# Kernel tuning notes

Measured on AMD Instinct MI355X. Metric: run time of the kernel, lower is better.

The kernel has to match this reference:

```python
import jax, jax.numpy as jnp
import numpy as np

DECAY = 0.99
EPSILON = 1e-05
CODEBOOK_SIZE = 1024


def setup_inputs() -> dict:
    key = jax.random.key(0)
    k1, k2, k3 = jax.random.split(key, 3)
    B, T, D, K = 8, 4096, 128, CODEBOOK_SIZE
    return {
        "x": jax.random.normal(k1, (B, T, D), dtype=jnp.float32),
        "embed": jax.random.normal(k2, (K, D), dtype=jnp.float32),
        "cluster_size": jnp.ones((K,), dtype=jnp.float32),
        "embed_avg": jax.random.normal(k3, (K, D), dtype=jnp.float32),
    }


def reference(x, embed, cluster_size, embed_avg):
    shape = x.shape
    K, D = embed.shape
    flat = x.reshape(-1, D)  # (N, D)

    dist = 2.0 * (flat @ embed.T) - jnp.sum(flat * flat, axis=1, keepdims=True) \
           - jnp.sum(embed * embed, axis=1)[None, :]  # (N, K)
    embed_ind_flat = jnp.argmax(dist, axis=-1)  # (N,) int
    embed_ind = embed_ind_flat.reshape(shape[:-1])
    quantize = embed[embed_ind]  # dequantize via gather, (B, T, D)

    # training EMA updates (one-hot scatter expressed as segment sums)
    counts = jax.ops.segment_sum(jnp.ones_like(embed_ind_flat, dtype=x.dtype),
                                 embed_ind_flat, num_segments=K)  # == onehot.sum(0)
    embed_sum = jax.ops.segment_sum(flat, embed_ind_flat, num_segments=K)  # == (x.T @ onehot).T

    new_cluster_size = cluster_size * DECAY + (1.0 - DECAY) * counts
    new_embed_avg = embed_avg * DECAY + (1.0 - DECAY) * embed_sum

    total = new_cluster_size.sum()
    smoothed = (new_cluster_size + EPSILON) / (total + K * EPSILON) * total
    new_embed = new_embed_avg / smoothed[:, None]

    return quantize, embed_ind, new_cluster_size, new_embed_avg, new_embed
```

## Files before the change

kernel.cpp:

```cpp
#include <hip/hip_runtime.h>

#define NROWS 32768
#define DDIM  128
#define KCODES 1024
#define DECAY 0.99f
#define OMD   0.01f
#define EPS   1e-5f

typedef __attribute__((ext_vector_type(8))) short short8;
typedef __attribute__((ext_vector_type(4))) float f32x4;

#define WS_COUNTS 0
#define WS_OFFS   1024
#define WS_CURSOR 2048
#define WS_INV    3072
#define WS_EN2H   4096
#define WS_BUCKET 5120

__device__ __forceinline__ unsigned int f2bf(float f) {
  union { float f; unsigned int u; } cv; cv.f = f;
  unsigned int u = cv.u;
  return (u + 0x7fffu + ((u >> 16) & 1u)) >> 16;
}

__global__ __launch_bounds__(256) void pack_e(const float* __restrict__ embed,
                                              ushort* __restrict__ epack,
                                              float* __restrict__ en2h) {
  const int tid = threadIdx.x;
  const int w = tid >> 6, lane = tid & 63;
  const int nt = blockIdx.x * 4 + w;
  const int m = lane & 15, q = lane >> 4;
  const int row = nt * 16 + m;
  const float* ep = embed + (size_t)row * DDIM + q * 8;
  float ss = 0.f;
  #pragma unroll
  for (int kb = 0; kb < 4; ++kb) {
    float4 v0 = *(const float4*)(ep + kb * 32);
    float4 v1 = *(const float4*)(ep + kb * 32 + 4);
    float v[8] = {v0.x, v0.y, v0.z, v0.w, v1.x, v1.y, v1.z, v1.w};
    unsigned int h[8], l[8];
    #pragma unroll
    for (int j = 0; j < 8; ++j) {
      ss += v[j] * v[j];
      h[j] = f2bf(v[j]);
      float fh = __uint_as_float(h[j] << 16);
      l[j] = f2bf(v[j] - fh);
    }
    uint4 ph, pl;
    ph.x = h[0] | (h[1] << 16); ph.y = h[2] | (h[3] << 16);
    ph.z = h[4] | (h[5] << 16); ph.w = h[6] | (h[7] << 16);
    pl.x = l[0] | (l[1] << 16); pl.y = l[2] | (l[3] << 16);
    pl.z = l[4] | (l[5] << 16); pl.w = l[6] | (l[7] << 16);
    *(uint4*)(epack + (((size_t)nt * 8 + kb) * 64 + lane) * 8)     = ph;
    *(uint4*)(epack + (((size_t)nt * 8 + kb + 4) * 64 + lane) * 8) = pl;
  }
  ss += __shfl_xor(ss, 16, 64);
  ss += __shfl_xor(ss, 32, 64);
  if (q == 0) en2h[row] = 0.5f * ss;
}

__global__ __launch_bounds__(256) void vq_mfma(
    const float* __restrict__ x, const short8* __restrict__ ep8,
    const float* __restrict__ en2h, const float* __restrict__ embed,
    float* __restrict__ out_ind, float* __restrict__ out_q) {
  __shared__ unsigned long long keys[4][32];
  __shared__ int scodes[32];
  const int tid = threadIdx.x;
  const int w = tid >> 6, lane = tid & 63;
  const int c = lane & 15, q = lane >> 4;
  const int mt0 = blockIdx.x * 2;

  short8 a[2][8];
  #pragma unroll
  for (int t = 0; t < 2; ++t) {
    const float* xp = x + (size_t)((mt0 + t) * 16 + c) * DDIM + q * 8;
    #pragma unroll
    for (int kb = 0; kb < 4; ++kb) {
      float4 v0 = *(const float4*)(xp + kb * 32);
      float4 v1 = *(const float4*)(xp + kb * 32 + 4);
      float v[8] = {v0.x, v0.y, v0.z, v0.w, v1.x, v1.y, v1.z, v1.w};
      short8 hh, ll;
      #pragma unroll
      for (int j = 0; j < 8; ++j) {
        unsigned int hv = f2bf(v[j]);
        hh[j] = (short)hv;
        float fh = __uint_as_float(hv << 16);
        ll[j] = (short)f2bf(v[j] - fh);
      }
      a[t][kb] = hh;
      a[t][kb + 4] = ll;
    }
  }

  float bestv[8]; int besti[8];
  #pragma unroll
  for (int i = 0; i < 8; ++i) { bestv[i] = -3.4e38f; besti[i] = 0; }

  const int nt0 = w * 16;
  for (int ch = 0; ch < 16; ++ch) {
    const int nt = nt0 + ch;
    short8 st[8];
    #pragma unroll
    for (int j = 0; j < 8; ++j)
      st[j] = ep8[((size_t)nt * 8 + j) * 64 + lane];
    const float nh = en2h[nt * 16 + c];
    f32x4 acc0 = {0.f, 0.f, 0.f, 0.f}, acc1 = {0.f, 0.f, 0.f, 0.f};
    #pragma unroll
    for (int kb = 0; kb < 4; ++kb) {
      acc0 = __builtin_amdgcn_mfma_f32_16x16x32_bf16(a[0][kb], st[kb], acc0, 0, 0, 0);
      acc1 = __builtin_amdgcn_mfma_f32_16x16x32_bf16(a[1][kb], st[kb], acc1, 0, 0, 0);
    }
    #pragma unroll
    for (int kb = 0; kb < 4; ++kb) {
      acc0 = __builtin_amdgcn_mfma_f32_16x16x32_bf16(a[0][kb + 4], st[kb], acc0, 0, 0, 0);
      acc1 = __builtin_amdgcn_mfma_f32_16x16x32_bf16(a[1][kb + 4], st[kb], acc1, 0, 0, 0);
    }
    #pragma unroll
    for (int kb = 0; kb < 4; ++kb) {
      acc0 = __builtin_amdgcn_mfma_f32_16x16x32_bf16(a[0][kb], st[kb + 4], acc0, 0, 0, 0);
      acc1 = __builtin_amdgcn_mfma_f32_16x16x32_bf16(a[1][kb], st[kb + 4], acc1, 0, 0, 0);
    }
    const int code = nt * 16 + c;
    #pragma unroll
    for (int r = 0; r < 4; ++r) {
      float s0 = acc0[r] - nh;
      if (s0 > bestv[r])     { bestv[r] = s0;     besti[r] = code; }
      float s1 = acc1[r] - nh;
      if (s1 > bestv[4 + r]) { bestv[4 + r] = s1; besti[4 + r] = code; }
    }
  }

  #pragma unroll
  for (int off = 1; off < 16; off <<= 1) {
    #pragma unroll
    for (int i = 0; i < 8; ++i) {
      float ov = __shfl_xor(bestv[i], off, 64);
      int   oi = __shfl_xor(besti[i], off, 64);
      if (ov > bestv[i] || (ov == bestv[i] && oi < besti[i])) {
        bestv[i] = ov; besti[i] = oi;
      }
    }
  }
  if (c == 0) {
    #pragma unroll
    for (int t = 0; t < 2; ++t)
      #pragma unroll
      for (int r = 0; r < 4; ++r) {
        unsigned u = __float_as_uint(bestv[t * 4 + r]);
        unsigned su = (u & 0x80000000u) ? ~u : (u | 0x80000000u);
        keys[w][t * 16 + q * 4 + r] =
            ((unsigned long long)su << 32) |
            (unsigned long long)(0xFFFFFFFFu - (unsigned)besti[t * 4 + r]);
      }
  }
  __syncthreads();
  if (tid < 32) {
    unsigned long long k0 = keys[0][tid], k1 = keys[1][tid];
    unsigned long long k2 = keys[2][tid], k3 = keys[3][tid];
    unsigned long long k = k0 > k1 ? k0 : k1;
    if (k2 > k) k = k2;
    if (k3 > k) k = k3;
    int code = (int)(0xFFFFFFFFu - (unsigned)(k & 0xFFFFFFFFull));
    out_ind[blockIdx.x * 32 + tid] = (float)code;
    scodes[tid] = code;
  }
  __syncthreads();
  #pragma unroll
  for (int it = 0; it < 4; ++it) {
    int idx = tid + it * 256;
    int row = idx >> 5, c4 = idx & 31;
    int code = scodes[row];
    *(float4*)(out_q + (size_t)(blockIdx.x * 32 + row) * DDIM + c4 * 4) =
        *(const float4*)(embed + (size_t)code * DDIM + c4 * 4);
  }
}

__global__ __launch_bounds__(1024) void scan_fin(
    const float* __restrict__ out_ind, const float* __restrict__ cs,
    float* __restrict__ counts_g, int* __restrict__ offs, int* __restrict__ cursor,
    float* __restrict__ inv, float* __restrict__ out_ncs) {
  __shared__ int hist[1024];
  __shared__ float wtot[16], ctot[16];
  const int tid = threadIdx.x;
  const int lane = tid & 63, w = tid >> 6;
  hist[tid] = 0;
  __syncthreads();
  #pragma unroll
  for (int i = 0; i < 32; ++i)
    atomicAdd(&hist[(int)out_ind[i * 1024 + tid]], 1);
  __syncthreads();
  const int cnt = hist[tid];
  const float cnum = (float)cnt;
  const float cv = cs[tid];
  float s = cnum;
  #pragma unroll
  for (int off = 1; off < 64; off <<= 1) {
    float v = __shfl_up(s, off, 64);
    if (lane >= off) s += v;
  }
  float r2 = cv;
  #pragma unroll
  for (int off = 32; off > 0; off >>= 1) r2 += __shfl_down(r2, off, 64);
  if (lane == 63) wtot[w] = s;
  if (lane == 0)  ctot[w] = r2;
  __syncthreads();
  if (tid < 16) {
    float v = wtot[tid];
    #pragma unroll
    for (int off = 1; off < 16; off <<= 1) {
      float p = __shfl_up(v, off, 64);
      if (tid >= off) v += p;
    }
    wtot[tid] = v;
    float t2 = ctot[tid];
    #pragma unroll
    for (int off = 8; off > 0; off >>= 1) t2 += __shfl_down(t2, off, 64);
    if (tid == 0) ctot[0] = t2;
  }
  __syncthreads();
  const float prefix = (w > 0) ? wtot[w - 1] : 0.f;
  const int excl = (int)(s + prefix) - cnt;
  offs[tid] = excl;
  cursor[tid] = excl;
  counts_g[tid] = cnum;
  const float ncs = cv * DECAY + OMD * cnum;
  out_ncs[tid] = ncs;
  const float total = ctot[0] * DECAY + OMD * (float)NROWS;
  inv[tid] = (total + (float)KCODES * EPS) / ((ncs + EPS) * total);
}

__global__ void scatter_rows(const float* __restrict__ out_ind,
                             int* __restrict__ cursor, int* __restrict__ bucket) {
  int row = blockIdx.x * 256 + threadIdx.x;
  int code = (int)out_ind[row];
  int pos = atomicAdd(cursor + code, 1);
  bucket[pos] = row;
}

__global__ __launch_bounds__(256) void esum_fin(
    const int* __restrict__ bucket, const int* __restrict__ offs,
    const float* __restrict__ counts, const float* __restrict__ x,
    const float* __restrict__ ea, const float* __restrict__ inv,
    float* __restrict__ out_nea, float* __restrict__ out_ne) {
  __shared__ float4 part[512];
  const int code = blockIdx.x;
  const int t = threadIdx.x;
  const int c8 = t & 15;
  const int h = t >> 4;
  const int start = offs[code];
  const int cnt = (int)counts[code];
  float4 a0 = {0.f, 0.f, 0.f, 0.f}, a1 = {0.f, 0.f, 0.f, 0.f};
  int i = h;
  for (; i + 16 < cnt; i += 32) {
    int rowA = bucket[start + i];
    int rowB = bucket[start + i + 16];
    const float* pa = x + (size_t)rowA * DDIM + c8 * 8;
    const float* pb = x + (size_t)rowB * DDIM + c8 * 8;
    float4 xa0 = *(const float4*)(pa), xa1 = *(const float4*)(pa + 4);
    float4 xb0 = *(const float4*)(pb), xb1 = *(const float4*)(pb + 4);
    a0.x += xa0.x + xb0.x; a0.y += xa0.y + xb0.y; a0.z += xa0.z + xb0.z; a0.w += xa0.w + xb0.w;
    a1.x += xa1.x + xb1.x; a1.y += xa1.y + xb1.y; a1.z += xa1.z + xb1.z; a1.w += xa1.w + xb1.w;
  }
  for (; i < cnt; i += 16) {
    int row = bucket[start + i];
    const float* pa = x + (size_t)row * DDIM + c8 * 8;
    float4 xa0 = *(const float4*)(pa), xa1 = *(const float4*)(pa + 4);
    a0.x += xa0.x; a0.y += xa0.y; a0.z += xa0.z; a0.w += xa0.w;
    a1.x += xa1.x; a1.y += xa1.y; a1.z += xa1.z; a1.w += xa1.w;
  }
  part[h * 32 + c8 * 2]     = a0;
  part[h * 32 + c8 * 2 + 1] = a1;
  __syncthreads();
  if (t < 32) {
    float4 s = part[t];
    #pragma unroll
    for (int hh = 1; hh < 16; ++hh) {
      float4 p = part[hh * 32 + t];
      s.x += p.x; s.y += p.y; s.z += p.z; s.w += p.w;
    }
    float iv = inv[code];
    int base = code * DDIM + t * 4;
    float4 a = *(const float4*)(ea + base);
    float4 nea;
    nea.x = a.x * DECAY + OMD * s.x; nea.y = a.y * DECAY + OMD * s.y;
    nea.z = a.z * DECAY + OMD * s.z; nea.w = a.w * DECAY + OMD * s.w;
    *(float4*)(out_nea + base) = nea;
    float4 ne;
    ne.x = nea.x * iv; ne.y = nea.y * iv; ne.z = nea.z * iv; ne.w = nea.w * iv;
    *(float4*)(out_ne + base) = ne;
  }
}

extern "C" void kernel_launch(void* const* d_in, const int* in_sizes, int n_in,
                              void* d_out, int out_size, void* d_ws, size_t ws_size,
                              hipStream_t stream) {
  const float* x     = (const float*)d_in[0];
  const float* embed = (const float*)d_in[1];
  const float* cs    = (const float*)d_in[2];
  const float* ea    = (const float*)d_in[3];

  float* out     = (float*)d_out;
  float* out_q   = out;
  float* out_ind = out_q + 4194304;
  float* out_ncs = out_ind + 32768;
  float* out_nea = out_ncs + 1024;
  float* out_ne  = out_nea + 131072;

  float* ws     = (float*)d_ws;
  float* counts = ws + WS_COUNTS;
  int*   offs   = (int*)(ws + WS_OFFS);
  int*   cursor = (int*)(ws + WS_CURSOR);
  float* inv    = ws + WS_INV;
  float* en2h   = ws + WS_EN2H;
  int*   bucket = (int*)(ws + WS_BUCKET);

  ushort* epack = (ushort*)out_nea;

  pack_e<<<16, 256, 0, stream>>>(embed, epack, en2h);
  vq_mfma<<<NROWS / 32, 256, 0, stream>>>(x, (const short8*)epack, en2h, embed,
                                          out_ind, out_q);
  scan_fin<<<1, 1024, 0, stream>>>(out_ind, cs, counts, offs, cursor, inv, out_ncs);
  scatter_rows<<<NROWS / 256, 256, 0, stream>>>(out_ind, cursor, bucket);
  esum_fin<<<KCODES, 256, 0, stream>>>(bucket, offs, counts, x, ea, inv,
                                       out_nea, out_ne);
}
```

Measured before the change: 170.2 us.

## Double-buffer codebook loads in VQ MFMA loop and fuse histogram via global atomics

Software-pipelines the codebook tile loads in the MFMA argmax loop with two register buffers, sched barriers and s_setprio around the MFMA block. The accumulator is now initialised with the negative half-norm, which drops a subtraction per element. The per-code histogram moves out of the single-block scan kernel into global atomics issued by the VQ kernel, with pack_e zeroing the counts. This removes the serial 32K-element shared-memory histogram pass, at the cost of contended global atomics and extra register pressure.

```diff
diff --git a/kernel.cpp b/kernel.cpp
--- a/kernel.cpp
+++ b/kernel.cpp
@@ -25,8 +25,13 @@
 
 __global__ __launch_bounds__(256) void pack_e(const float* __restrict__ embed,
                                               ushort* __restrict__ epack,
-                                              float* __restrict__ en2h) {
+                                              float* __restrict__ en2h,
+                                              int* __restrict__ cnt0) {
   const int tid = threadIdx.x;
+  if (blockIdx.x == 0) {
+    #pragma unroll
+    for (int i = 0; i < 4; ++i) cnt0[tid + i * 256] = 0;
+  }
   const int w = tid >> 6, lane = tid & 63;
   const int nt = blockIdx.x * 4 + w;
   const int m = lane & 15, q = lane >> 4;
@@ -62,7 +67,8 @@
 __global__ __launch_bounds__(256) void vq_mfma(
     const float* __restrict__ x, const short8* __restrict__ ep8,
     const float* __restrict__ en2h, const float* __restrict__ embed,
-    float* __restrict__ out_ind, float* __restrict__ out_q) {
+    float* __restrict__ out_ind, float* __restrict__ out_q,
+    int* __restrict__ cnt_i) {
   __shared__ unsigned long long keys[4][32];
   __shared__ int scodes[32];
   const int tid = threadIdx.x;
@@ -97,14 +103,13 @@
   for (int i = 0; i < 8; ++i) { bestv[i] = -3.4e38f; besti[i] = 0; }
 
   const int nt0 = w * 16;
-  for (int ch = 0; ch < 16; ++ch) {
-    const int nt = nt0 + ch;
-    short8 st[8];
-    #pragma unroll
-    for (int j = 0; j < 8; ++j)
-      st[j] = ep8[((size_t)nt * 8 + j) * 64 + lane];
-    const float nh = en2h[nt * 16 + c];
-    f32x4 acc0 = {0.f, 0.f, 0.f, 0.f}, acc1 = {0.f, 0.f, 0.f, 0.f};
+  const short8* pb = ep8 + (size_t)nt0 * 8 * 64 + lane;
+  const float* pn = en2h + nt0 * 16 + c;
+
+  auto proc = [&](const short8 (&st)[8], float nh, int nt) {
+    f32x4 acc0 = {-nh, -nh, -nh, -nh};
+    f32x4 acc1 = acc0;
+    __builtin_amdgcn_s_setprio(1);
     #pragma unroll
     for (int kb = 0; kb < 4; ++kb) {
       acc0 = __builtin_amdgcn_mfma_f32_16x16x32_bf16(a[0][kb], st[kb], acc0, 0, 0, 0);
@@ -120,15 +125,42 @@
       acc0 = __builtin_amdgcn_mfma_f32_16x16x32_bf16(a[0][kb], st[kb + 4], acc0, 0, 0, 0);
       acc1 = __builtin_amdgcn_mfma_f32_16x16x32_bf16(a[1][kb], st[kb + 4], acc1, 0, 0, 0);
     }
+    __builtin_amdgcn_s_setprio(0);
     const int code = nt * 16 + c;
     #pragma unroll
     for (int r = 0; r < 4; ++r) {
-      float s0 = acc0[r] - nh;
-      if (s0 > bestv[r])     { bestv[r] = s0;     besti[r] = code; }
-      float s1 = acc1[r] - nh;
-      if (s1 > bestv[4 + r]) { bestv[4 + r] = s1; besti[4 + r] = code; }
-    }
-  }
+      if (acc0[r] > bestv[r])     { bestv[r] = acc0[r];     besti[r] = code; }
+      if (acc1[r] > bestv[4 + r]) { bestv[4 + r] = acc1[r]; besti[4 + r] = code; }
+    }
+  };
+
+  short8 sA[8], sB[8];
+  float nhA, nhB;
+  #pragma unroll
+  for (int j = 0; j < 8; ++j) sA[j] = pb[j * 64];
+  nhA = pn[0];
+
+  for (int ch = 0; ch < 14; ch += 2) {
+    pb += 512;
+    #pragma unroll
+    for (int j = 0; j < 8; ++j) sB[j] = pb[j * 64];
+    nhB = pn[16 * (ch + 1)];
+    __builtin_amdgcn_sched_barrier(0);
+    proc(sA, nhA, nt0 + ch);
+    pb += 512;
+    #pragma unroll
+    for (int j = 0; j < 8; ++j) sA[j] = pb[j * 64];
+    nhA = pn[16 * (ch + 2)];
+    __builtin_amdgcn_sched_barrier(0);
+    proc(sB, nhB, nt0 + ch + 1);
+  }
+  pb += 512;
+  #pragma unroll
+  for (int j = 0; j < 8; ++j) sB[j] = pb[j * 64];
+  nhB = pn[16 * 15];
+  __builtin_amdgcn_sched_barrier(0);
+  proc(sA, nhA, nt0 + 14);
+  proc(sB, nhB, nt0 + 15);
 
   #pragma unroll
   for (int off = 1; off < 16; off <<= 1) {
@@ -163,6 +195,7 @@
     int code = (int)(0xFFFFFFFFu - (unsigned)(k & 0xFFFFFFFFull));
     out_ind[blockIdx.x * 32 + tid] = (float)code;
     scodes[tid] = code;
+    atomicAdd(&cnt_i[code], 1);
   }
   __syncthreads();
   #pragma unroll
@@ -176,20 +209,13 @@
 }
 
 __global__ __launch_bounds__(1024) void scan_fin(
-    const float* __restrict__ out_ind, const float* __restrict__ cs,
-    float* __restrict__ counts_g, int* __restrict__ offs, int* __restrict__ cursor,
+    int* offs, const float* __restrict__ cs,
+    float* __restrict__ counts_g, int* __restrict__ cursor,
     float* __restrict__ inv, float* __restrict__ out_ncs) {
-  __shared__ int hist[1024];
   __shared__ float wtot[16], ctot[16];
   const int tid = threadIdx.x;
   const int lane = tid & 63, w = tid >> 6;
-  hist[tid] = 0;
-  __syncthreads();
-  #pragma unroll
-  for (int i = 0; i < 32; ++i)
-    atomicAdd(&hist[(int)out_ind[i * 1024 + tid]], 1);
-  __syncthreads();
-  const int cnt = hist[tid];
+  const int cnt = offs[tid];
   const float cnum = (float)cnt;
   const float cv = cs[tid];
   float s = cnum;
@@ -316,10 +342,10 @@
 
   ushort* epack = (ushort*)out_nea;
 
-  pack_e<<<16, 256, 0, stream>>>(embed, epack, en2h);
+  pack_e<<<16, 256, 0, stream>>>(embed, epack, en2h, offs);
   vq_mfma<<<NROWS / 32, 256, 0, stream>>>(x, (const short8*)epack, en2h, embed,
-                                          out_ind, out_q);
-  scan_fin<<<1, 1024, 0, stream>>>(out_ind, cs, counts, offs, cursor, inv, out_ncs);
+                                          out_ind, out_q, offs);
+  scan_fin<<<1, 1024, 0, stream>>>(offs, cs, counts, cursor, inv, out_ncs);
   scatter_rows<<<NROWS / 256, 256, 0, stream>>>(out_ind, cursor, bucket);
   esum_fin<<<KCODES, 256, 0, stream>>>(bucket, offs, counts, x, ea, inv,
                                        out_nea, out_ne);
```

Result: faster. 161.2 us (-5.3%).

## Restructure VQ kernel to stage codebook in LDS and fuse histogram

Applied to the files above, without the earlier changes.

The nearest-code kernel now uses 512-thread blocks covering 128 rows. Each wave holds one 16-row A tile and sweeps all 1024 codes instead of splitting codes across waves. Codebook fragments are double-buffered into LDS via global_load_lds, and the half-norms are staged in LDS and folded into the accumulator init. The three split-bf16 MFMA chains are interleaved into independent accumulators, and the cross-wave argmax reduction disappears. Code counts are now accumulated with global atomics in the VQ kernel, zeroed in pack_e, which removes the single-block histogram pass in scan_fin but adds per-iteration barriers and atomic contention.

```diff
diff --git a/kernel.cpp b/kernel.cpp
--- a/kernel.cpp
+++ b/kernel.cpp
@@ -23,57 +23,72 @@
   return (u + 0x7fffu + ((u >> 16) & 1u)) >> 16;
 }
 
+__device__ __forceinline__ void gload16(const void* g, void* l) {
+  __builtin_amdgcn_global_load_lds(
+      (const __attribute__((address_space(1))) unsigned int*)g,
+      (__attribute__((address_space(3))) unsigned int*)l, 16, 0, 0);
+}
+
 __global__ __launch_bounds__(256) void pack_e(const float* __restrict__ embed,
                                               ushort* __restrict__ epack,
-                                              float* __restrict__ en2h) {
+                                              float* __restrict__ en2h,
+                                              int* __restrict__ cnt0) {
   const int tid = threadIdx.x;
-  const int w = tid >> 6, lane = tid & 63;
-  const int nt = blockIdx.x * 4 + w;
-  const int m = lane & 15, q = lane >> 4;
+  const int nt = blockIdx.x;
+  if (nt == 0) {
+    #pragma unroll
+    for (int i = 0; i < 4; ++i) cnt0[tid + i * 256] = 0;
+  }
+  const int m = tid >> 4, s = tid & 15;
+  const int kb = s >> 2, q = s & 3;
   const int row = nt * 16 + m;
-  const float* ep = embed + (size_t)row * DDIM + q * 8;
+  const float* ep = embed + (size_t)row * DDIM + kb * 32 + q * 8;
+  float4 v0 = *(const float4*)(ep);
+  float4 v1 = *(const float4*)(ep + 4);
+  float v[8] = {v0.x, v0.y, v0.z, v0.w, v1.x, v1.y, v1.z, v1.w};
+  unsigned int h[8], l[8];
   float ss = 0.f;
   #pragma unroll
-  for (int kb = 0; kb < 4; ++kb) {
-    float4 v0 = *(const float4*)(ep + kb * 32);
-    float4 v1 = *(const float4*)(ep + kb * 32 + 4);
-    float v[8] = {v0.x, v0.y, v0.z, v0.w, v1.x, v1.y, v1.z, v1.w};
-    unsigned int h[8], l[8];
-    #pragma unroll
-    for (int j = 0; j < 8; ++j) {
-      ss += v[j] * v[j];
-      h[j] = f2bf(v[j]);
-      float fh = __uint_as_float(h[j] << 16);
-      l[j] = f2bf(v[j] - fh);
-    }
-    uint4 ph, pl;
-    ph.x = h[0] | (h[1] << 16); ph.y = h[2] | (h[3] << 16);
-    ph.z = h[4] | (h[5] << 16); ph.w = h[6] | (h[7] << 16);
-    pl.x = l[0] | (l[1] << 16); pl.y = l[2] | (l[3] << 16);
-    pl.z = l[4] | (l[5] << 16); pl.w = l[6] | (l[7] << 16);
-    *(uint4*)(epack + (((size_t)nt * 8 + kb) * 64 + lane) * 8)     = ph;
-    *(uint4*)(epack + (((size_t)nt * 8 + kb + 4) * 64 + lane) * 8) = pl;
-  }
-  ss += __shfl_xor(ss, 16, 64);
-  ss += __shfl_xor(ss, 32, 64);
-  if (q == 0) en2h[row] = 0.5f * ss;
-}
-
-__global__ __launch_bounds__(256) void vq_mfma(
+  for (int j = 0; j < 8; ++j) {
+    ss += v[j] * v[j];
+    h[j] = f2bf(v[j]);
+    float fh = __uint_as_float(h[j] << 16);
+    l[j] = f2bf(v[j] - fh);
+  }
+  uint4 ph, pl;
+  ph.x = h[0] | (h[1] << 16); ph.y = h[2] | (h[3] << 16);
+  ph.z = h[4] | (h[5] << 16); ph.w = h[6] | (h[7] << 16);
+  pl.x = l[0] | (l[1] << 16); pl.y = l[2] | (l[3] << 16);
+  pl.z = l[4] | (l[5] << 16); pl.w = l[6] | (l[7] << 16);
+  *(uint4*)(epack + (((size_t)nt * 8 + kb) * 64 + q * 16 + m) * 8)     = ph;
+  *(uint4*)(epack + (((size_t)nt * 8 + kb + 4) * 64 + q * 16 + m) * 8) = pl;
+  ss += __shfl_xor(ss, 1, 64);
+  ss += __shfl_xor(ss, 2, 64);
+  ss += __shfl_xor(ss, 4, 64);
+  ss += __shfl_xor(ss, 8, 64);
+  if (s == 0) en2h[row] = 0.5f * ss;
+}
+
+__global__ __launch_bounds__(512, 2) void vq_mfma(
     const float* __restrict__ x, const short8* __restrict__ ep8,
     const float* __restrict__ en2h, const float* __restrict__ embed,
-    float* __restrict__ out_ind, float* __restrict__ out_q) {
-  __shared__ unsigned long long keys[4][32];
-  __shared__ int scodes[32];
+    float* __restrict__ out_ind, float* __restrict__ out_q,
+    int* __restrict__ cnt_i) {
+  __shared__ short8 bfrag[2][512];
+  __shared__ float nlds[KCODES];
+  __shared__ int scodes[128];
   const int tid = threadIdx.x;
   const int w = tid >> 6, lane = tid & 63;
   const int c = lane & 15, q = lane >> 4;
-  const int mt0 = blockIdx.x * 2;
-
-  short8 a[2][8];
-  #pragma unroll
-  for (int t = 0; t < 2; ++t) {
-    const float* xp = x + (size_t)((mt0 + t) * 16 + c) * DDIM + q * 8;
+  const int row0 = blockIdx.x * 128;
+
+  gload16(ep8 + w * 64 + lane, &bfrag[0][w * 64]);
+  nlds[tid]       = en2h[tid];
+  nlds[tid + 512] = en2h[tid + 512];
+
+  short8 a[8];
+  {
+    const float* xp = x + (size_t)(row0 + w * 16 + c) * DDIM + q * 8;
     #pragma unroll
     for (int kb = 0; kb < 4; ++kb) {
       float4 v0 = *(const float4*)(xp + kb * 32);
@@ -87,53 +102,57 @@
         float fh = __uint_as_float(hv << 16);
         ll[j] = (short)f2bf(v[j] - fh);
       }
-      a[t][kb] = hh;
-      a[t][kb + 4] = ll;
-    }
-  }
-
-  float bestv[8]; int besti[8];
-  #pragma unroll
-  for (int i = 0; i < 8; ++i) { bestv[i] = -3.4e38f; besti[i] = 0; }
-
-  const int nt0 = w * 16;
-  for (int ch = 0; ch < 16; ++ch) {
-    const int nt = nt0 + ch;
+      a[kb] = hh;
+      a[kb + 4] = ll;
+    }
+  }
+
+  float bestv[4]; int besti[4];
+  #pragma unroll
+  for (int i = 0; i < 4; ++i) { bestv[i] = -3.4e38f; besti[i] = 0; }
+
+  asm volatile("s_waitcnt vmcnt(0)" ::: "memory");
+  __syncthreads();
+
+  for (int nt = 0; nt < 64; ++nt) {
+    const int cur = nt & 1;
+    if (nt < 63)
+      gload16(ep8 + (size_t)(nt + 1) * 512 + w * 64 + lane,
+              &bfrag[cur ^ 1][w * 64]);
+    __builtin_amdgcn_sched_barrier(0);
+
     short8 st[8];
     #pragma unroll
-    for (int j = 0; j < 8; ++j)
-      st[j] = ep8[((size_t)nt * 8 + j) * 64 + lane];
-    const float nh = en2h[nt * 16 + c];
-    f32x4 acc0 = {0.f, 0.f, 0.f, 0.f}, acc1 = {0.f, 0.f, 0.f, 0.f};
+    for (int j = 0; j < 8; ++j) st[j] = bfrag[cur][j * 64 + lane];
+    const float nh = nlds[nt * 16 + c];
+
+    f32x4 accA = {-nh, -nh, -nh, -nh};
+    f32x4 accB = {0.f, 0.f, 0.f, 0.f};
+    f32x4 accC = {0.f, 0.f, 0.f, 0.f};
+    __builtin_amdgcn_s_setprio(1);
     #pragma unroll
     for (int kb = 0; kb < 4; ++kb) {
-      acc0 = __builtin_amdgcn_mfma_f32_16x16x32_bf16(a[0][kb], st[kb], acc0, 0, 0, 0);
-      acc1 = __builtin_amdgcn_mfma_f32_16x16x32_bf16(a[1][kb], st[kb], acc1, 0, 0, 0);
-    }
-    #pragma unroll
-    for (int kb = 0; kb < 4; ++kb) {
-      acc0 = __builtin_amdgcn_mfma_f32_16x16x32_bf16(a[0][kb + 4], st[kb], acc0, 0, 0, 0);
-      acc1 = __builtin_amdgcn_mfma_f32_16x16x32_bf16(a[1][kb + 4], st[kb], acc1, 0, 0, 0);
-    }
-    #pragma unroll
-    for (int kb = 0; kb < 4; ++kb) {
-      acc0 = __builtin_amdgcn_mfma_f32_16x16x32_bf16(a[0][kb], st[kb + 4], acc0, 0, 0, 0);
-      acc1 = __builtin_amdgcn_mfma_f32_16x16x32_bf16(a[1][kb], st[kb + 4], acc1, 0, 0, 0);
-    }
+      accA = __builtin_amdgcn_mfma_f32_16x16x32_bf16(a[kb],     st[kb],     accA, 0, 0, 0);
+      accB = __builtin_amdgcn_mfma_f32_16x16x32_bf16(a[kb + 4], st[kb],     accB, 0, 0, 0);
+      accC = __builtin_amdgcn_mfma_f32_16x16x32_bf16(a[kb],     st[kb + 4], accC, 0, 0, 0);
+    }
+    __builtin_amdgcn_s_setprio(0);
+
     const int code = nt * 16 + c;
     #pragma unroll
     for (int r = 0; r < 4; ++r) {
-      float s0 = acc0[r] - nh;
-      if (s0 > bestv[r])     { bestv[r] = s0;     besti[r] = code; }
-      float s1 = acc1[r] - nh;
-      if (s1 > bestv[4 + r]) { bestv[4 + r] = s1; besti[4 + r] = code; }
-    }
+      float s = accA[r] + accB[r] + accC[r];
+      if (s > bestv[r]) { bestv[r] = s; besti[r] = code; }
+    }
+
+    asm volatile("s_waitcnt vmcnt(0)" ::: "memory");
+    __syncthreads();
   }
 
   #pragma unroll
   for (int off = 1; off < 16; off <<= 1) {
     #pragma unroll
-    for (int i = 0; i < 8; ++i) {
+    for (int i = 0; i < 4; ++i) {
       float ov = __shfl_xor(bestv[i], off, 64);
       int   oi = __shfl_xor(besti[i], off, 64);
       if (ov > bestv[i] || (ov == bestv[i] && oi < besti[i])) {
@@ -143,53 +162,32 @@
   }
   if (c == 0) {
     #pragma unroll
-    for (int t = 0; t < 2; ++t)
-      #pragma unroll
-      for (int r = 0; r < 4; ++r) {
-        unsigned u = __float_as_uint(bestv[t * 4 + r]);
-        unsigned su = (u & 0x80000000u) ? ~u : (u | 0x80000000u);
-        keys[w][t * 16 + q * 4 + r] =
-            ((unsigned long long)su << 32) |
-            (unsigned long long)(0xFFFFFFFFu - (unsigned)besti[t * 4 + r]);
-      }
-  }
-  __syncthreads();
-  if (tid < 32) {
-    unsigned long long k0 = keys[0][tid], k1 = keys[1][tid];
-    unsigned long long k2 = keys[2][tid], k3 = keys[3][tid];
-    unsigned long long k = k0 > k1 ? k0 : k1;
-    if (k2 > k) k = k2;
-    if (k3 > k) k = k3;
-    int code = (int)(0xFFFFFFFFu - (unsigned)(k & 0xFFFFFFFFull));
-    out_ind[blockIdx.x * 32 + tid] = (float)code;
-    scodes[tid] = code;
-  }
-  __syncthreads();
-  #pragma unroll
-  for (int it = 0; it < 4; ++it) {
-    int idx = tid + it * 256;
+    for (int r = 0; r < 4; ++r) {
+      const int row = w * 16 + q * 4 + r;
+      out_ind[row0 + row] = (float)besti[r];
+      scodes[row] = besti[r];
+      atomicAdd(&cnt_i[besti[r]], 1);
+    }
+  }
+  __syncthreads();
+  #pragma unroll
+  for (int it = 0; it < 8; ++it) {
+    int idx = tid + it * 512;
     int row = idx >> 5, c4 = idx & 31;
     int code = scodes[row];
-    *(float4*)(out_q + (size_t)(blockIdx.x * 32 + row) * DDIM + c4 * 4) =
+    *(float4*)(out_q + (size_t)(row0 + row) * DDIM + c4 * 4) =
         *(const float4*)(embed + (size_t)code * DDIM + c4 * 4);
   }
 }
 
 __global__ __launch_bounds__(1024) void scan_fin(
-    const float* __restrict__ out_ind, const float* __restrict__ cs,
-    float* __restrict__ counts_g, int* __restrict__ offs, int* __restrict__ cursor,
+    int* offs, const float* __restrict__ cs,
+    float* __restrict__ counts_g, int* __restrict__ cursor,
     float* __restrict__ inv, float* __restrict__ out_ncs) {
-  __shared__ int hist[1024];
   __shared__ float wtot[16], ctot[16];
   const int tid = threadIdx.x;
   const int lane = tid & 63, w = tid >> 6;
-  hist[tid] = 0;
-  __syncthreads();
-  #pragma unroll
-  for (int i = 0; i < 32; ++i)
-    atomicAdd(&hist[(int)out_ind[i * 1024 + tid]], 1);
-  __syncthreads();
-  const int cnt = hist[tid];
+  const int cnt = offs[tid];
   const float cnum = (float)cnt;
   const float cv = cs[tid];
   float s = cnum;
@@ -316,10 +314,10 @@
 
   ushort* epack = (ushort*)out_nea;
 
-  pack_e<<<16, 256, 0, stream>>>(embed, epack, en2h);
-  vq_mfma<<<NROWS / 32, 256, 0, stream>>>(x, (const short8*)epack, en2h, embed,
-                                          out_ind, out_q);
-  scan_fin<<<1, 1024, 0, stream>>>(out_ind, cs, counts, offs, cursor, inv, out_ncs);
+  pack_e<<<64, 256, 0, stream>>>(embed, epack, en2h, offs);
+  vq_mfma<<<NROWS / 128, 512, 0, stream>>>(x, (const short8*)epack, en2h, embed,
+                                           out_ind, out_q, offs);
+  scan_fin<<<1, 1024, 0, stream>>>(offs, cs, counts, cursor, inv, out_ncs);
   scatter_rows<<<NROWS / 256, 256, 0, stream>>>(out_ind, cursor, bucket);
   esum_fin<<<KCODES, 256, 0, stream>>>(bucket, offs, counts, x, ea, inv,
                                        out_nea, out_ne);
```

Result: slower. 187.2 us (+10.0%).
